# Performance work log

Measured on AMD Instinct MI355X. Metric: run time of the kernel, lower is better.

## Reference

```python
import jax, jax.numpy as jnp
import numpy as np

BETA_2 = 1.0
LAMBDA_2 = 1.0


def _segment_logsumexp(x, seg, num_segments):
    # numerically stable segment logsumexp; empty segments -> 0.0
    m = jax.ops.segment_max(x, seg, num_segments=num_segments)
    m_safe = jnp.where(jnp.isfinite(m), m, 0.0)
    s = jax.ops.segment_sum(jnp.exp(x - m_safe[seg]), seg, num_segments=num_segments)
    lse = m_safe + jnp.log(s)
    return jnp.where(s > 0, lse, 0.0)


def setup_inputs() -> dict:
    key = jax.random.key(0)
    k1, k2, k3, k4, k5 = jax.random.split(key, 5)
    num_nodes, d, num_edges, num_graphs = 100000, 64, 3200000, 256
    Q2 = jax.random.normal(k1, (num_nodes, d), dtype=jnp.float32)
    K2 = jax.random.normal(k2, (num_nodes, d), dtype=jnp.float32)
    c_2 = jax.random.randint(k3, (num_edges,), 0, num_nodes)
    u_2 = jax.random.randint(k4, (num_edges,), 0, num_nodes)
    batch = jnp.sort(jax.random.randint(k5, (num_nodes,), 0, num_graphs))
    return {"Q2": Q2, "K2": K2, "c_2": c_2, "u_2": u_2, "batch": batch,
            "num_graphs": num_graphs}


def reference(Q2, K2, c_2, u_2, batch, num_graphs):
    num_nodes, d = Q2.shape
    scale = d ** 0.5
    # pairwise dot over edges: [E]
    ell_2 = jnp.sum(Q2[c_2] * K2[u_2], axis=-1) / scale
    # segment logsumexp grouped by destination node c: [N]
    lse_2 = _segment_logsumexp(BETA_2 * ell_2, c_2, num_nodes)
    # scatter-add per-node lse into per-graph energy: [G]
    graph_lse = jax.ops.segment_sum(lse_2, batch, num_segments=num_graphs)
    E = (LAMBDA_2 / BETA_2) * graph_lse
    return E
```

## Files before the change

### kernel.cpp

```cpp
#include <hip/hip_runtime.h>
#include <hip/hip_fp8.h>
#include <math.h>

typedef __attribute__((ext_vector_type(2))) float fv2;

#if defined(__has_builtin)
#  if __has_builtin(__builtin_amdgcn_cvt_pk_f32_fp8) && \
      __has_builtin(__builtin_amdgcn_cvt_pk_fp8_f32)
#    define PE_HAVE_FP8_BUILTINS 1
#  endif
#endif

#define MAX_NB 1024
#define NPB 256
#define NPB_SHIFT 8
#define B2_EPT 16
#define B2_CHUNK (B2_EPT * 256)
#define CPB 4
#define RT 1024

__device__ __forceinline__ unsigned pack4_fp8(float a, float b, float c, float d) {
#ifdef PE_HAVE_FP8_BUILTINS
    int w = 0;
    w = __builtin_amdgcn_cvt_pk_fp8_f32(a, b, w, false);
    w = __builtin_amdgcn_cvt_pk_fp8_f32(c, d, w, true);
    return (unsigned)w;
#else
    unsigned r = 0;
    r |= (unsigned)__hip_fp8_e4m3(a).__x;
    r |= (unsigned)__hip_fp8_e4m3(b).__x << 8;
    r |= (unsigned)__hip_fp8_e4m3(c).__x << 16;
    r |= (unsigned)__hip_fp8_e4m3(d).__x << 24;
    return r;
#endif
}

__device__ __forceinline__ float dot4w_fp8(unsigned qa, unsigned ka, float acc) {
#ifdef PE_HAVE_FP8_BUILTINS
    fv2 q0 = __builtin_amdgcn_cvt_pk_f32_fp8((int)qa, false);
    fv2 q1 = __builtin_amdgcn_cvt_pk_f32_fp8((int)qa, true);
    fv2 k0 = __builtin_amdgcn_cvt_pk_f32_fp8((int)ka, false);
    fv2 k1 = __builtin_amdgcn_cvt_pk_f32_fp8((int)ka, true);
    acc = fmaf(q0.x, k0.x, acc);
    acc = fmaf(q0.y, k0.y, acc);
    acc = fmaf(q1.x, k1.x, acc);
    acc = fmaf(q1.y, k1.y, acc);
    return acc;
#else
#pragma unroll
    for (int j = 0; j < 4; ++j) {
        __hip_fp8_e4m3 qv, kv;
        qv.__x = (qa >> (8 * j)) & 0xff;
        kv.__x = (ka >> (8 * j)) & 0xff;
        acc = fmaf((float)qv, (float)kv, acc);
    }
    return acc;
#endif
}

__device__ __forceinline__ float dot16_fp8(const uint4& q, const uint4& k) {
    float d = 0.0f;
    d = dot4w_fp8(q.x, k.x, d);
    d = dot4w_fp8(q.y, k.y, d);
    d = dot4w_fp8(q.z, k.z, d);
    d = dot4w_fp8(q.w, k.w, d);
    return d;
}

__device__ __forceinline__ float red4(float d) {
    d += __shfl_xor(d, 1, 64);
    d += __shfl_xor(d, 2, 64);
    return d;
}

__global__ __launch_bounds__(256) void pe_convert_kernel(
    const float* __restrict__ Q,
    const float* __restrict__ K,
    unsigned* __restrict__ Qq,
    unsigned* __restrict__ Kq,
    float* __restrict__ node_sum,
    unsigned* __restrict__ bucket_cnt,
    float* __restrict__ out,
    int n4,
    int num_nodes,
    int num_graphs) {
    const int i = blockIdx.x * blockDim.x + threadIdx.x;
    if (i < num_nodes) node_sum[i] = 0.0f;
    if (bucket_cnt && i < MAX_NB) bucket_cnt[i] = 0u;
    if (i < num_graphs) out[i] = 0.0f;
    if (i >= n4) return;

    const float4 q = ((const float4*)Q)[i];
    const float4 k = ((const float4*)K)[i];
    Qq[i] = pack4_fp8(q.x, q.y, q.z, q.w);
    Kq[i] = pack4_fp8(k.x, k.y, k.z, k.w);
}

__global__ __launch_bounds__(256) void pe_hist_kernel(
    const int* __restrict__ c,
    unsigned* __restrict__ bucket_cnt,
    int num_edges, int nb) {
    __shared__ unsigned h[MAX_NB];
    const int tid = threadIdx.x;
    for (int b = tid; b < nb; b += 256) h[b] = 0u;
    __syncthreads();

    const int stride = gridDim.x * blockDim.x;
    const int gid = blockIdx.x * blockDim.x + tid;
    const int E4 = num_edges >> 2;
    for (int k = gid; k < E4; k += stride) {
        const int4 v = ((const int4*)c)[k];
        atomicAdd(&h[v.x >> NPB_SHIFT], 1u);
        atomicAdd(&h[v.y >> NPB_SHIFT], 1u);
        atomicAdd(&h[v.z >> NPB_SHIFT], 1u);
        atomicAdd(&h[v.w >> NPB_SHIFT], 1u);
    }
    for (int e = (E4 << 2) + gid; e < num_edges; e += stride)
        atomicAdd(&h[c[e] >> NPB_SHIFT], 1u);
    __syncthreads();

    for (int b = tid; b < nb; b += 256)
        if (h[b]) atomicAdd(&bucket_cnt[b], h[b]);
}

__global__ __launch_bounds__(1024) void pe_scan_kernel(
    const unsigned* __restrict__ bucket_cnt,
    unsigned* __restrict__ bucket_base,
    unsigned* __restrict__ gcursor,
    int nb) {
    __shared__ unsigned s[MAX_NB];
    const int t = threadIdx.x;
    const unsigned v = (t < nb) ? bucket_cnt[t] : 0u;
    s[t] = v;
    __syncthreads();
    for (int off = 1; off < MAX_NB; off <<= 1) {
        const unsigned mine = s[t];
        const unsigned add = (t >= off) ? s[t - off] : 0u;
        __syncthreads();
        s[t] = mine + add;
        __syncthreads();
    }
    const unsigned excl = s[t] - v;
    if (t < nb) {
        bucket_base[t] = excl;
        gcursor[t] = excl;
    }
    if (t == 0) bucket_base[nb] = s[MAX_NB - 1];
}

__global__ __launch_bounds__(256) void pe_binify_kernel(
    const int* __restrict__ c,
    const int* __restrict__ u,
    unsigned* __restrict__ gcursor,
    unsigned* __restrict__ recs,
    int num_edges, int nb) {
    __shared__ unsigned cnt[MAX_NB];
    __shared__ unsigned basesh[MAX_NB];

    const int tid = threadIdx.x;
    const int estart = blockIdx.x * B2_CHUNK;

    for (int b = tid; b < nb; b += 256) cnt[b] = 0u;
    __syncthreads();

    unsigned rw[B2_EPT];
    int rb[B2_EPT];
    int rr[B2_EPT];

#pragma unroll
    for (int j = 0; j < B2_EPT; ++j) {
        rb[j] = -1;
        const int e = estart + j * 256 + tid;
        if (e < num_edges) {
            const int cc = c[e];
            const int uu = u[e];
            rb[j] = cc >> NPB_SHIFT;
            rw[j] = ((unsigned)uu << NPB_SHIFT) | (unsigned)(cc & (NPB - 1));
            rr[j] = (int)atomicAdd(&cnt[rb[j]], 1u);
        }
    }
    __syncthreads();

    for (int b = tid; b < nb; b += 256) {
        const unsigned n = cnt[b];
        basesh[b] = n ? atomicAdd(&gcursor[b], n) : 0u;
    }
    __syncthreads();

#pragma unroll
    for (int j = 0; j < B2_EPT; ++j) {
        if (rb[j] >= 0) recs[basesh[rb[j]] + (unsigned)rr[j]] = rw[j];
    }
}

__global__ __launch_bounds__(256) void pe_dotred_kernel(
    const unsigned* __restrict__ Qq,
    const unsigned* __restrict__ Kq,
    const unsigned* __restrict__ recs,
    const unsigned* __restrict__ bucket_base,
    float* __restrict__ node_sum,
    int num_nodes) {
    __shared__ uint4 qlds[NPB * 4];
    __shared__ float acc[NPB];
    __shared__ unsigned rlds[RT];

    const int B = blockIdx.x / CPB;
    const int chunk = blockIdx.x - B * CPB;
    const int t = threadIdx.x;
    const int g = t >> 2;
    const int sub = t & 3;
    const float inv_scale = 0.125f;

    const int nrows = min(NPB, num_nodes - B * NPB);
    const uint4* qsrc = (const uint4*)Qq + (size_t)B * NPB * 4;
    for (int i = t; i < nrows * 4; i += 256) qlds[i] = qsrc[i];
    acc[t] = 0.0f;

    const unsigned s0 = bucket_base[B];
    const unsigned len = bucket_base[B + 1] - s0;
    const unsigned r0 = s0 + (unsigned)(((unsigned long long)len * chunk) / CPB);
    const unsigned r1 = s0 + (unsigned)(((unsigned long long)len * (chunk + 1)) / CPB);

    for (unsigned t0 = r0; t0 < r1; t0 += RT) {
        const unsigned n = min((unsigned)RT, r1 - t0);
        __syncthreads();
        for (unsigned i = t; i < n; i += 256) rlds[i] = recs[t0 + i];
        __syncthreads();
        for (unsigned i = g; i < n; i += 64) {
            const unsigned rec = rlds[i];
            const unsigned uu = rec >> NPB_SHIFT;
            const unsigned local = rec & (NPB - 1);
            const uint4 k = *(const uint4*)(Kq + (size_t)uu * 16 + sub * 4);
            const uint4 q = qlds[local * 4 + sub];
            const float d = red4(dot16_fp8(q, k));
            if (sub == 0) atomicAdd(&acc[local], __expf(d * inv_scale));
        }
    }
    __syncthreads();

    if (t < nrows && acc[t] != 0.0f)
        atomicAdd(&node_sum[B * NPB + t], acc[t]);
}

__global__ __launch_bounds__(256) void pe_node_kernel(
    const float* __restrict__ node_sum,
    const int* __restrict__ batch,
    float* __restrict__ out,
    int num_nodes) {
    const int n = blockIdx.x * blockDim.x + threadIdx.x;
    const bool valid = (n < num_nodes);
    const int nc = valid ? n : (num_nodes - 1);

    const float s = valid ? node_sum[nc] : 0.0f;
    float lse = (s > 0.0f) ? logf(s) : 0.0f;
    if (!valid) lse = 0.0f;
    const int b = batch[nc];

    const int b0 = __shfl(b, 0, 64);
    const bool uniform = __all(b == b0);
    if (uniform) {
        lse += __shfl_xor(lse, 1, 64);
        lse += __shfl_xor(lse, 2, 64);
        lse += __shfl_xor(lse, 4, 64);
        lse += __shfl_xor(lse, 8, 64);
        lse += __shfl_xor(lse, 16, 64);
        lse += __shfl_xor(lse, 32, 64);
        if ((threadIdx.x & 63) == 0 && lse != 0.0f) {
            atomicAdd(&out[b0], lse);
        }
    } else {
        if (valid && lse != 0.0f) {
            atomicAdd(&out[b], lse);
        }
    }
}


__global__ __launch_bounds__(256) void pe_edge_kernel(
    const unsigned* __restrict__ Qq,
    const unsigned* __restrict__ Kq,
    const int* __restrict__ c,
    const int* __restrict__ u,
    float* __restrict__ node_sum,
    int num_edges) {
    const int tid = blockIdx.x * blockDim.x + threadIdx.x;
    const int group = tid >> 2;
    const int sub = tid & 3;
    const int ngroups = (gridDim.x * blockDim.x) >> 2;
    const float inv_scale = 0.125f;

    const int E4 = num_edges & ~3;

    for (int base = group * 4; base < E4; base += ngroups * 4) {
        const int4 ci = *(const int4*)(c + base);
        const int4 ui = *(const int4*)(u + base);

        const uint4 q0 = *(const uint4*)(Qq + (size_t)ci.x * 16 + sub * 4);
        const uint4 q1 = *(const uint4*)(Qq + (size_t)ci.y * 16 + sub * 4);
        const uint4 q2 = *(const uint4*)(Qq + (size_t)ci.z * 16 + sub * 4);
        const uint4 q3 = *(const uint4*)(Qq + (size_t)ci.w * 16 + sub * 4);
        const uint4 k0 = *(const uint4*)(Kq + (size_t)ui.x * 16 + sub * 4);
        const uint4 k1 = *(const uint4*)(Kq + (size_t)ui.y * 16 + sub * 4);
        const uint4 k2 = *(const uint4*)(Kq + (size_t)ui.z * 16 + sub * 4);
        const uint4 k3 = *(const uint4*)(Kq + (size_t)ui.w * 16 + sub * 4);

        float d0 = red4(dot16_fp8(q0, k0));
        float d1 = red4(dot16_fp8(q1, k1));
        float d2 = red4(dot16_fp8(q2, k2));
        float d3 = red4(dot16_fp8(q3, k3));

        const float dsel = (sub == 0) ? d0 : (sub == 1) ? d1 : (sub == 2) ? d2 : d3;
        const int csel = (sub == 0) ? ci.x : (sub == 1) ? ci.y : (sub == 2) ? ci.z : ci.w;
        atomicAdd(&node_sum[csel], __expf(dsel * inv_scale));
    }

    for (int e = E4 + group; e < num_edges; e += ngroups) {
        const int cc = c[e];
        const int uu = u[e];
        const uint4 q = *(const uint4*)(Qq + (size_t)cc * 16 + sub * 4);
        const uint4 k = *(const uint4*)(Kq + (size_t)uu * 16 + sub * 4);
        float d = red4(dot16_fp8(q, k));
        if (sub == 0) atomicAdd(&node_sum[cc], __expf(d * inv_scale));
    }
}

extern "C" void kernel_launch(void* const* d_in, const int* in_sizes, int n_in,
                              void* d_out, int out_size, void* d_ws, size_t ws_size,
                              hipStream_t stream) {
    const float* Q2 = (const float*)d_in[0];
    const float* K2 = (const float*)d_in[1];
    const int* c_2 = (const int*)d_in[2];
    const int* u_2 = (const int*)d_in[3];
    const int* batch = (const int*)d_in[4];

    const int num_nodes = in_sizes[4];
    const int num_edges = in_sizes[2];
    const int num_graphs = out_size;
    const int d = in_sizes[0] / num_nodes;
    const size_t row_elems = (size_t)num_nodes * d;
    const size_t row_bytes = row_elems;

    unsigned* Qq = (unsigned*)d_ws;
    unsigned* Kq = Qq + row_bytes / 4;
    unsigned* meta = Kq + row_bytes / 4;
    unsigned* bucket_cnt = meta;
    unsigned* bucket_base = meta + MAX_NB;
    unsigned* gcursor = bucket_base + MAX_NB + 1;
    float* node_sum_b = (float*)(meta + 3 * MAX_NB + 16);
    const size_t ns_pad = ((size_t)num_nodes + 15) & ~(size_t)15;
    unsigned* recs = (unsigned*)node_sum_b + ns_pad;
    float* node_sum_f = (float*)meta;
    float* out = (float*)d_out;

    const int nb = (num_nodes + NPB - 1) >> NPB_SHIFT;
    const size_t need_binned = row_bytes * 2 + (size_t)(3 * MAX_NB + 16) * 4 +
                               ns_pad * 4 + (size_t)num_edges * 4;
    const bool use_binned = (nb <= MAX_NB) && (ws_size >= need_binned) &&
                            (d == 64) && (num_nodes <= (1 << 24));

    float* node_sum = use_binned ? node_sum_b : node_sum_f;

    {
        const int n4 = (int)(row_elems / 4);
        const int block = 256;
        const int grid = (n4 + block - 1) / block;
        pe_convert_kernel<<<grid, block, 0, stream>>>(
            Q2, K2, Qq, Kq, node_sum,
            use_binned ? bucket_cnt : nullptr,
            out, n4, num_nodes, num_graphs);
    }

    if (use_binned) {
        pe_hist_kernel<<<256, 256, 0, stream>>>(c_2, bucket_cnt, num_edges, nb);
        pe_scan_kernel<<<1, 1024, 0, stream>>>(bucket_cnt, bucket_base, gcursor, nb);
        {
            const int grid = (num_edges + B2_CHUNK - 1) / B2_CHUNK;
            pe_binify_kernel<<<grid, 256, 0, stream>>>(c_2, u_2, gcursor, recs,
                                                       num_edges, nb);
        }
        pe_dotred_kernel<<<nb * CPB, 256, 0, stream>>>(Qq, Kq, recs, bucket_base,
                                                       node_sum, num_nodes);
    } else {
        pe_edge_kernel<<<8192, 256, 0, stream>>>(Qq, Kq, c_2, u_2,
                                                 node_sum, num_edges);
    }

    {
        const int block = 256;
        const int grid = (num_nodes + block - 1) / block;
        pe_node_kernel<<<grid, block, 0, stream>>>(node_sum, batch, out,
                                                   num_nodes);
    }
}
```

Before: 228.2 us.

## Replace global-atomic bucket cursors with per-block count matrix and scan

The bucket histogram is now computed per edge chunk into a bucket-by-block count matrix, which a new per-bucket scan kernel turns into deterministic per-block offsets. The binify kernel then reads its offsets directly instead of reserving space with global atomics on shared cursors. It also uses int4 loads for full chunks, and the dotred kernel is split into twice as many chunks per bucket. The cost is one extra kernel launch and a count matrix of roughly 391x782 entries written and read back.

Result: faster. 216.1 us (-5.3%).

```diff
diff --git a/kernel.cpp b/kernel.cpp
--- a/kernel.cpp
+++ b/kernel.cpp
@@ -16,7 +16,7 @@
 #define NPB_SHIFT 8
 #define B2_EPT 16
 #define B2_CHUNK (B2_EPT * 256)
-#define CPB 4
+#define CPB 8
 #define RT 1024
 
 __device__ __forceinline__ unsigned pack4_fp8(float a, float b, float c, float d) {
@@ -79,14 +79,12 @@
     unsigned* __restrict__ Qq,
     unsigned* __restrict__ Kq,
     float* __restrict__ node_sum,
-    unsigned* __restrict__ bucket_cnt,
     float* __restrict__ out,
     int n4,
     int num_nodes,
     int num_graphs) {
     const int i = blockIdx.x * blockDim.x + threadIdx.x;
     if (i < num_nodes) node_sum[i] = 0.0f;
-    if (bucket_cnt && i < MAX_NB) bucket_cnt[i] = 0u;
     if (i < num_graphs) out[i] = 0.0f;
     if (i >= n4) return;
 
@@ -96,37 +94,65 @@
     Kq[i] = pack4_fp8(k.x, k.y, k.z, k.w);
 }
 
-__global__ __launch_bounds__(256) void pe_hist_kernel(
+__global__ __launch_bounds__(256) void pe_count_kernel(
     const int* __restrict__ c,
-    unsigned* __restrict__ bucket_cnt,
-    int num_edges, int nb) {
+    unsigned* __restrict__ cnt_mat,
+    int num_edges, int nb, int nblk) {
     __shared__ unsigned h[MAX_NB];
     const int tid = threadIdx.x;
+    const int blk = blockIdx.x;
     for (int b = tid; b < nb; b += 256) h[b] = 0u;
     __syncthreads();
 
-    const int stride = gridDim.x * blockDim.x;
-    const int gid = blockIdx.x * blockDim.x + tid;
-    const int E4 = num_edges >> 2;
-    for (int k = gid; k < E4; k += stride) {
-        const int4 v = ((const int4*)c)[k];
+    const int estart = blk * B2_CHUNK;
+    const int ecount = min(B2_CHUNK, num_edges - estart);
+    const int n4 = ecount >> 2;
+    const int4* c4 = (const int4*)(c + estart);
+    for (int k = tid; k < n4; k += 256) {
+        const int4 v = c4[k];
         atomicAdd(&h[v.x >> NPB_SHIFT], 1u);
         atomicAdd(&h[v.y >> NPB_SHIFT], 1u);
         atomicAdd(&h[v.z >> NPB_SHIFT], 1u);
         atomicAdd(&h[v.w >> NPB_SHIFT], 1u);
     }
-    for (int e = (E4 << 2) + gid; e < num_edges; e += stride)
-        atomicAdd(&h[c[e] >> NPB_SHIFT], 1u);
+    for (int e = (n4 << 2) + tid; e < ecount; e += 256)
+        atomicAdd(&h[c[estart + e] >> NPB_SHIFT], 1u);
     __syncthreads();
 
     for (int b = tid; b < nb; b += 256)
-        if (h[b]) atomicAdd(&bucket_cnt[b], h[b]);
+        cnt_mat[(size_t)b * nblk + blk] = h[b];
+}
+
+__global__ __launch_bounds__(256) void pe_matscan_kernel(
+    unsigned* __restrict__ cnt_mat,
+    unsigned* __restrict__ bucket_cnt,
+    int nblk) {
+    __shared__ unsigned s[256];
+    const int t = threadIdx.x;
+    unsigned* row = cnt_mat + (size_t)blockIdx.x * nblk;
+    unsigned carry = 0u;
+    for (int t0 = 0; t0 < nblk; t0 += 256) {
+        const int i = t0 + t;
+        const unsigned v = (i < nblk) ? row[i] : 0u;
+        s[t] = v;
+        __syncthreads();
+        for (int off = 1; off < 256; off <<= 1) {
+            const unsigned mine = s[t];
+            const unsigned add = (t >= off) ? s[t - off] : 0u;
+            __syncthreads();
+            s[t] = mine + add;
+            __syncthreads();
+        }
+        if (i < nblk) row[i] = carry + (s[t] - v);
+        carry += s[255];
+        __syncthreads();
+    }
+    if (t == 0) bucket_cnt[blockIdx.x] = carry;
 }
 
 __global__ __launch_bounds__(1024) void pe_scan_kernel(
     const unsigned* __restrict__ bucket_cnt,
     unsigned* __restrict__ bucket_base,
-    unsigned* __restrict__ gcursor,
     int nb) {
     __shared__ unsigned s[MAX_NB];
     const int t = threadIdx.x;
@@ -140,56 +166,75 @@
         s[t] = mine + add;
         __syncthreads();
     }
-    const unsigned excl = s[t] - v;
-    if (t < nb) {
-        bucket_base[t] = excl;
-        gcursor[t] = excl;
-    }
+    if (t < nb) bucket_base[t] = s[t] - v;
     if (t == 0) bucket_base[nb] = s[MAX_NB - 1];
 }
 
 __global__ __launch_bounds__(256) void pe_binify_kernel(
     const int* __restrict__ c,
     const int* __restrict__ u,
-    unsigned* __restrict__ gcursor,
+    const unsigned* __restrict__ cnt_mat,
+    const unsigned* __restrict__ bucket_base,
     unsigned* __restrict__ recs,
-    int num_edges, int nb) {
-    __shared__ unsigned cnt[MAX_NB];
+    int num_edges, int nb, int nblk) {
+    __shared__ unsigned rank[MAX_NB];
     __shared__ unsigned basesh[MAX_NB];
 
     const int tid = threadIdx.x;
-    const int estart = blockIdx.x * B2_CHUNK;
-
-    for (int b = tid; b < nb; b += 256) cnt[b] = 0u;
+    const int blk = blockIdx.x;
+    const int estart = blk * B2_CHUNK;
+    const int ecount = min(B2_CHUNK, num_edges - estart);
+
+    for (int b = tid; b < nb; b += 256) {
+        rank[b] = 0u;
+        basesh[b] = bucket_base[b] + cnt_mat[(size_t)b * nblk + blk];
+    }
     __syncthreads();
 
     unsigned rw[B2_EPT];
     int rb[B2_EPT];
-    int rr[B2_EPT];
+    unsigned rr[B2_EPT];
+
+    if (ecount == B2_CHUNK) {
+        const int4* c4 = (const int4*)(c + estart);
+        const int4* u4 = (const int4*)(u + estart);
+#pragma unroll
+        for (int jj = 0; jj < 4; ++jj) {
+            const int k = jj * 256 + tid;
+            const int4 cv = c4[k];
+            const int4 uv = u4[k];
+            const int j = jj * 4;
+            rb[j + 0] = cv.x >> NPB_SHIFT;
+            rb[j + 1] = cv.y >> NPB_SHIFT;
+            rb[j + 2] = cv.z >> NPB_SHIFT;
+            rb[j + 3] = cv.w >> NPB_SHIFT;
+            rw[j + 0] = ((unsigned)uv.x << NPB_SHIFT) | (unsigned)(cv.x & (NPB - 1));
+            rw[j + 1] = ((unsigned)uv.y << NPB_SHIFT) | (unsigned)(cv.y & (NPB - 1));
+            rw[j + 2] = ((unsigned)uv.z << NPB_SHIFT) | (unsigned)(cv.z & (NPB - 1));
+            rw[j + 3] = ((unsigned)uv.w << NPB_SHIFT) | (unsigned)(cv.w & (NPB - 1));
+            rr[j + 0] = atomicAdd(&rank[rb[j + 0]], 1u);
+            rr[j + 1] = atomicAdd(&rank[rb[j + 1]], 1u);
+            rr[j + 2] = atomicAdd(&rank[rb[j + 2]], 1u);
+            rr[j + 3] = atomicAdd(&rank[rb[j + 3]], 1u);
+        }
+    } else {
+#pragma unroll
+        for (int j = 0; j < B2_EPT; ++j) {
+            rb[j] = -1;
+            const int e = estart + j * 256 + tid;
+            if (e < num_edges) {
+                const int cc = c[e];
+                const int uu = u[e];
+                rb[j] = cc >> NPB_SHIFT;
+                rw[j] = ((unsigned)uu << NPB_SHIFT) | (unsigned)(cc & (NPB - 1));
+                rr[j] = atomicAdd(&rank[rb[j]], 1u);
+            }
+        }
+    }
 
 #pragma unroll
     for (int j = 0; j < B2_EPT; ++j) {
-        rb[j] = -1;
-        const int e = estart + j * 256 + tid;
-        if (e < num_edges) {
-            const int cc = c[e];
-            const int uu = u[e];
-            rb[j] = cc >> NPB_SHIFT;
-            rw[j] = ((unsigned)uu << NPB_SHIFT) | (unsigned)(cc & (NPB - 1));
-            rr[j] = (int)atomicAdd(&cnt[rb[j]], 1u);
-        }
-    }
-    __syncthreads();
-
-    for (int b = tid; b < nb; b += 256) {
-        const unsigned n = cnt[b];
-        basesh[b] = n ? atomicAdd(&gcursor[b], n) : 0u;
-    }
-    __syncthreads();
-
-#pragma unroll
-    for (int j = 0; j < B2_EPT; ++j) {
-        if (rb[j] >= 0) recs[basesh[rb[j]] + (unsigned)rr[j]] = rw[j];
+        if (rb[j] >= 0) recs[basesh[rb[j]] + rr[j]] = rw[j];
     }
 }
 
@@ -340,21 +385,24 @@
     const size_t row_elems = (size_t)num_nodes * d;
     const size_t row_bytes = row_elems;
 
+    const int nb = (num_nodes + NPB - 1) >> NPB_SHIFT;
+    const int nblk = (num_edges + B2_CHUNK - 1) / B2_CHUNK;
+
     unsigned* Qq = (unsigned*)d_ws;
     unsigned* Kq = Qq + row_bytes / 4;
     unsigned* meta = Kq + row_bytes / 4;
     unsigned* bucket_cnt = meta;
     unsigned* bucket_base = meta + MAX_NB;
-    unsigned* gcursor = bucket_base + MAX_NB + 1;
-    float* node_sum_b = (float*)(meta + 3 * MAX_NB + 16);
+    float* node_sum_b = (float*)(meta + 2 * MAX_NB + 16);
     const size_t ns_pad = ((size_t)num_nodes + 15) & ~(size_t)15;
     unsigned* recs = (unsigned*)node_sum_b + ns_pad;
+    unsigned* cnt_mat = recs + num_edges;
     float* node_sum_f = (float*)meta;
     float* out = (float*)d_out;
 
-    const int nb = (num_nodes + NPB - 1) >> NPB_SHIFT;
-    const size_t need_binned = row_bytes * 2 + (size_t)(3 * MAX_NB + 16) * 4 +
-                               ns_pad * 4 + (size_t)num_edges * 4;
+    const size_t need_binned = row_bytes * 2 + (size_t)(2 * MAX_NB + 16) * 4 +
+                               ns_pad * 4 + (size_t)num_edges * 4 +
+                               (size_t)nb * nblk * 4;
     const bool use_binned = (nb <= MAX_NB) && (ws_size >= need_binned) &&
                             (d == 64) && (num_nodes <= (1 << 24));
 
@@ -365,20 +413,19 @@
         const int block = 256;
         const int grid = (n4 + block - 1) / block;
         pe_convert_kernel<<<grid, block, 0, stream>>>(
-            Q2, K2, Qq, Kq, node_sum,
-            use_binned ? bucket_cnt : nullptr,
-            out, n4, num_nodes, num_graphs);
+            Q2, K2, Qq, Kq, node_sum, out, n4, num_nodes, num_graphs);
     }
 
     if (use_binned) {
-        pe_hist_kernel<<<256, 256, 0, stream>>>(c_2, bucket_cnt, num_edges, nb);
-        pe_scan_kernel<<<1, 1024, 0, stream>>>(bucket_cnt, bucket_base, gcursor, nb);
-        {
-            const int grid = (num_edges + B2_CHUNK - 1) / B2_CHUNK;
-            pe_binify_kernel<<<grid, 256, 0, stream>>>(c_2, u_2, gcursor, recs,
-                                                       num_edges, nb);
-        }
-        pe_dotred_kernel<<<nb * CPB, 256, 0, stream>>>(Qq, Kq, recs, bucket_base,
+        pe_count_kernel<<<nblk, 256, 0, stream>>>(c_2, cnt_mat,
+                                                  num_edges, nb, nblk);
+        pe_matscan_kernel<<<nb, 256, 0, stream>>>(cnt_mat, bucket_cnt, nblk);
+        pe_scan_kernel<<<1, 1024, 0, stream>>>(bucket_cnt, bucket_base, nb);
+        pe_binify_kernel<<<nblk, 256, 0, stream>>>(c_2, u_2, cnt_mat,
+                                                   bucket_base, recs,
+                                                   num_edges, nb, nblk);
+        pe_dotred_kernel<<<nb * CPB, 256, 0, stream>>>(Qq, Kq, recs,
+                                                       bucket_base,
                                                        node_sum, num_nodes);
     } else {
         pe_edge_kernel<<<8192, 256, 0, stream>>>(Qq, Kq, c_2, u_2,
```
